# Kernel tuning notes

Hardware: AMD Instinct MI355X
Metric: run time of the kernel (lower is better)

## Reference

```python
import jax, jax.numpy as jnp
import numpy as np

N_NODES = 50000
N_EDGES = 800000
F_IN = 32
H = 128
N_REL = 4
MAX_DEG = 10
N_GRAPHS = 64
N_BLOCKS = 2


def setup_inputs() -> dict:
    key = jax.random.key(0)
    ks = jax.random.split(key, 20)
    s = 0.05
    return {
        "x": jax.random.normal(ks[0], (N_NODES, F_IN), jnp.float32),
        "edge_index": jax.random.randint(ks[1], (2, N_EDGES), 0, N_NODES, dtype=jnp.int32),
        "edge_attr": jax.random.randint(ks[2], (N_EDGES,), 0, N_REL, dtype=jnp.int32),
        "batch_idx": jnp.sort(jax.random.randint(ks[3], (N_NODES,), 0, N_GRAPHS, dtype=jnp.int32)),
        "embed_W": jax.random.normal(ks[4], (F_IN, H), jnp.float32) * s,
        "embed_b": jax.random.normal(ks[5], (H,), jnp.float32) * s,
        "rgcn_Wrel": jax.random.normal(ks[6], (N_BLOCKS, N_REL, H, H), jnp.float32) * s,
        "rgcn_Wroot": jax.random.normal(ks[7], (N_BLOCKS, H, H), jnp.float32) * s,
        "rgcn_b": jax.random.normal(ks[8], (N_BLOCKS, H), jnp.float32) * s,
        "mf_Wl": jax.random.normal(ks[9], (N_BLOCKS, MAX_DEG + 1, H, H), jnp.float32) * s,
        "mf_bl": jax.random.normal(ks[10], (N_BLOCKS, MAX_DEG + 1, H), jnp.float32) * s,
        "mf_Wr": jax.random.normal(ks[11], (N_BLOCKS, MAX_DEG + 1, H, H), jnp.float32) * s,
        "lin1_W": jax.random.normal(ks[12], (H, H), jnp.float32) * s,
        "lin1_b": jax.random.normal(ks[13], (H,), jnp.float32) * s,
        "lin2_W": jax.random.normal(ks[14], (H, 1), jnp.float32) * s,
        "lin2_b": jax.random.normal(ks[15], (1,), jnp.float32) * s,
    }


def _rgcn(x, src, dst, rel, Wrel, Wroot, b):
    # PyG RGCNConv with default aggr='mean': per-relation mean over incoming
    # edges, then per-relation weight, plus root transform and bias.
    seg = dst * N_REL + rel  # composite segment id: (node, relation)
    agg = jax.ops.segment_sum(x[src], seg, num_segments=N_NODES * N_REL)
    cnt = jax.ops.segment_sum(jnp.ones((seg.shape[0],), x.dtype), seg,
                              num_segments=N_NODES * N_REL)
    agg = (agg / jnp.maximum(cnt, 1.0)[:, None]).reshape(N_NODES, N_REL, H)
    return jnp.einsum('nrh,rho->no', agg, Wrel) + x @ Wroot + b


def _mfconv(x, src, dst, Wl, bl, Wr):
    # PyG MFConv: sum-aggregate neighbors, then per-degree-bucket linear heads
    # (degree = in-degree clamped to MAX_DEG); lin_r applied to root x (no bias).
    h = jax.ops.segment_sum(x[src], dst, num_segments=N_NODES)  # [N,H]
    deg = jax.ops.segment_sum(jnp.ones((src.shape[0],), jnp.int32), dst,
                              num_segments=N_NODES)
    deg = jnp.minimum(deg, MAX_DEG)  # [N]
    # out_all: [D+1, N, H] candidate outputs, one per degree bucket
    out_all = (jnp.einsum('nh,dho->dno', h, Wl)
               + jnp.einsum('nh,dho->dno', x, Wr)
               + bl[:, None, :])
    return jnp.take_along_axis(out_all, deg[None, :, None], axis=0)[0]


def reference(x, edge_index, edge_attr, batch_idx, embed_W, embed_b,
              rgcn_Wrel, rgcn_Wroot, rgcn_b, mf_Wl, mf_bl, mf_Wr,
              lin1_W, lin1_b, lin2_W, lin2_b):
    src, dst = edge_index[0], edge_index[1]
    h = x @ embed_W + embed_b
    for blk in range(N_BLOCKS):
        if blk > 0:  # first block uses Identity instead of ReLU
            h = jax.nn.relu(h)
        h = _rgcn(h, src, dst, edge_attr, rgcn_Wrel[blk], rgcn_Wroot[blk], rgcn_b[blk])
        h = jax.nn.relu(h)
        h = _mfconv(h, src, dst, mf_Wl[blk], mf_bl[blk], mf_Wr[blk])
    g = jax.ops.segment_sum(h, batch_idx, num_segments=N_GRAPHS)  # global_add_pool
    g = jax.nn.relu(g @ lin1_W + lin1_b)
    return g @ lin2_W + lin2_b
```

## Files before the change

### kernel.cpp

```cpp
#include <hip/hip_runtime.h>
#include <hip/hip_bf16.h>

#define NRELS 4
#define MAXDEG 10
#define NBUCK 11
#define POOL_CHUNKS 8

typedef __attribute__((ext_vector_type(8))) short s16x8;
typedef __attribute__((ext_vector_type(4))) float f32x4;
typedef __attribute__((ext_vector_type(8))) unsigned short u16x8;

__device__ inline unsigned short f2b(float f) {
  __hip_bfloat16 h = __float2bfloat16(f);
  return *reinterpret_cast<unsigned short*>(&h);
}
__device__ inline float b2f(unsigned short u) {
  union { unsigned int i; float f; } v;
  v.i = ((unsigned int)u) << 16;
  return v.f;
}
__device__ inline float blo(unsigned int v) {
  union { unsigned int i; float f; } x;
  x.i = v << 16;
  return x.f;
}
__device__ inline float bhi(unsigned int v) {
  union { unsigned int i; float f; } x;
  x.i = v & 0xffff0000u;
  return x.f;
}

typedef __attribute__((address_space(3))) unsigned int lds_uint;
typedef __attribute__((address_space(1))) const unsigned int glob_uint;
__device__ __forceinline__ void gld_lds16(const void* g, void* l) {
  __builtin_amdgcn_global_load_lds((glob_uint*)g, (lds_uint*)l, 16, 0, 0);
}

__global__ __launch_bounds__(512) void coarse_count(const int* __restrict__ dst,
                                                    int* __restrict__ bhist, int E) {
  __shared__ int lh[512];
  int t = threadIdx.x;
  lh[t] = 0;
  __syncthreads();
  int base = blockIdx.x * 4096;
  int lim = E - base;
  if (lim > 4096) lim = 4096;
  for (int i = t; i < lim; i += 512) atomicAdd(&lh[dst[base + i] >> 7], 1);
  __syncthreads();
  if (lh[t]) atomicAdd(&bhist[t], lh[t]);
}

__global__ __launch_bounds__(512) void coarse_scan(const int* __restrict__ bhist,
                                                   int* __restrict__ boff,
                                                   int* __restrict__ bcur, int NB, int E) {
  __shared__ int sd[512];
  int t = threadIdx.x;
  int v = (t < NB) ? bhist[t] : 0;
  sd[t] = v;
  __syncthreads();
  for (int o = 1; o < 512; o <<= 1) {
    int x = (t >= o) ? sd[t - o] : 0;
    __syncthreads();
    sd[t] += x;
    __syncthreads();
  }
  if (t < NB) {
    int st = sd[t] - v;
    boff[t] = st;
    bcur[t] = st;
  }
  if (t == 0) boff[NB] = E;
}

__global__ __launch_bounds__(512) void coarse_scatter(
    const int* __restrict__ src, const int* __restrict__ dst, const int* __restrict__ rel,
    int* __restrict__ bcur, uint2* __restrict__ ebuf, int E) {
  __shared__ int lhist[512];
  __shared__ int lstart[512];
  __shared__ int lcur[512];
  __shared__ int gbase[512];
  __shared__ uint2 stage[4096];
  int t = threadIdx.x;
  lhist[t] = 0;
  __syncthreads();
  int base = blockIdx.x * 4096;
  int lim = E - base;
  if (lim > 4096) lim = 4096;
  for (int i = t; i < lim; i += 512) atomicAdd(&lhist[dst[base + i] >> 7], 1);
  __syncthreads();
  int myc = lhist[t];
  lstart[t] = myc;
  __syncthreads();
  for (int o = 1; o < 512; o <<= 1) {
    int x = (t >= o) ? lstart[t - o] : 0;
    __syncthreads();
    lstart[t] += x;
    __syncthreads();
  }
  int incl = lstart[t];
  __syncthreads();
  lstart[t] = incl - myc;
  lcur[t] = 0;
  if (myc > 0) gbase[t] = atomicAdd(&bcur[t], myc);
  __syncthreads();
  for (int i = t; i < lim; i += 512) {
    int e = base + i;
    int d = dst[e];
    int b = d >> 7;
    int slot = lstart[b] + atomicAdd(&lcur[b], 1);
    stage[slot] = make_uint2((unsigned)(d * 4 + rel[e]), (unsigned)src[e]);
  }
  __syncthreads();
  for (int i = t; i < lim; i += 512) {
    uint2 val = stage[i];
    int b = (int)(val.x >> 9);
    ebuf[gbase[b] + (i - lstart[b])] = val;
  }
}

__global__ __launch_bounds__(512) void fine_count(const uint2* __restrict__ ebuf,
                                                  const int* __restrict__ boff,
                                                  int* __restrict__ cnt, int NSEG) {
  __shared__ int lh[512];
  int t = threadIdx.x;
  int b = blockIdx.x;
  lh[t] = 0;
  __syncthreads();
  int s = boff[b], e = boff[b + 1];
  for (int i = s + t; i < e; i += 512) atomicAdd(&lh[ebuf[i].x & 511], 1);
  __syncthreads();
  int gseg = b * 512 + t;
  if (gseg < NSEG) cnt[gseg] = lh[t];
}

__global__ __launch_bounds__(512) void place_local(const uint2* __restrict__ ebuf,
                                                   const int* __restrict__ boff,
                                                   const int* __restrict__ seg_start,
                                                   int* __restrict__ csr, int NSEG) {
  __shared__ int lcur[512];
  int t = threadIdx.x;
  int b = blockIdx.x;
  int gseg = b * 512 + t;
  lcur[t] = (gseg < NSEG) ? seg_start[gseg] : 0;
  __syncthreads();
  int s = boff[b], e = boff[b + 1];
  for (int i = s + t; i < e; i += 512) {
    uint2 v = ebuf[i];
    int pos = atomicAdd(&lcur[v.x & 511], 1);
    csr[pos] = (int)v.y;
  }
}

__global__ void prep_nodes(const int* __restrict__ cnt, float* __restrict__ inv,
                           int* __restrict__ deg, int* __restrict__ bucket,
                           int* __restrict__ hist, int N) {
  int n = blockIdx.x * 256 + threadIdx.x;
  int b = -1;
  if (n < N) {
    int d = 0;
    for (int r = 0; r < 4; r++) {
      int c = cnt[n * 4 + r];
      d += c;
      inv[n * 4 + r] = 1.0f / (float)(c > 1 ? c : 1);
    }
    deg[n] = d;
    b = d < MAXDEG ? d : MAXDEG;
    bucket[n] = b;
  }
  int lane = threadIdx.x & 63;
  for (int bb = 0; bb < NBUCK; bb++) {
    unsigned long long m = __ballot(b == bb);
    if (m == 0ULL) continue;
    int leader = __ffsll(m) - 1;
    if (lane == leader) atomicAdd(&hist[bb], __popcll(m));
  }
}

__global__ void calc_offsets(const int* __restrict__ hist, int* __restrict__ off,
                             int* __restrict__ fill) {
  if (threadIdx.x == 0) {
    int acc = 0;
    for (int b = 0; b < NBUCK; b++) {
      off[b] = acc;
      fill[b] = acc;
      acc += ((hist[b] + 63) >> 6) << 6;
    }
    off[NBUCK] = acc;
  }
}

__global__ void build_perm(const int* __restrict__ bucket, int* __restrict__ fill,
                           int* __restrict__ perm, int N) {
  int n = blockIdx.x * 256 + threadIdx.x;
  int b = (n < N) ? bucket[n] : -1;
  int lane = threadIdx.x & 63;
  for (int bb = 0; bb < NBUCK; bb++) {
    unsigned long long m = __ballot(b == bb);
    if (m == 0ULL) continue;
    int leader = __ffsll(m) - 1;
    int base = 0;
    if (lane == leader) base = atomicAdd(&fill[bb], __popcll(m));
    base = __shfl(base, leader);
    if (b == bb) {
      int idx = __popcll(m & ((1ULL << lane) - 1ULL));
      perm[base + idx] = n;
    }
  }
}

__global__ void assign_segments(const int* __restrict__ cnt, int* __restrict__ seg_start,
                                int* __restrict__ cursor, int NSEG) {
  __shared__ int sd[256];
  __shared__ int sbase;
  int t = threadIdx.x;
  int s = blockIdx.x * 256 + t;
  int v = (s < NSEG) ? cnt[s] : 0;
  sd[t] = v;
  __syncthreads();
  for (int o = 1; o < 256; o <<= 1) {
    int x = (t >= o) ? sd[t - o] : 0;
    __syncthreads();
    sd[t] += x;
    __syncthreads();
  }
  if (t == 255) sbase = atomicAdd(cursor, sd[255]);
  __syncthreads();
  if (s < NSEG) seg_start[s] = sbase + sd[t] - v;
}

__global__ void conv_weights(const float* __restrict__ Wrel, const float* __restrict__ Wroot,
                             const float* __restrict__ Wl, const float* __restrict__ Wr,
                             unsigned short* __restrict__ Bt, unsigned short* __restrict__ Btm) {
  int t = blockIdx.x * 256 + threadIdx.x;
  if (t < 2 * 128 * 640) {
    int blk = t / 81920;
    int rem = t % 81920;
    int n = rem / 640;
    int k = rem % 640;
    float v;
    if (k < 512)
      v = Wrel[(size_t)blk * 65536 + (size_t)k * 128 + n];
    else
      v = Wroot[(size_t)blk * 16384 + (size_t)(k - 512) * 128 + n];
    Bt[t] = f2b(v);
    return;
  }
  int t2 = t - 2 * 128 * 640;
  if (t2 >= 2 * 11 * 128 * 256) return;
  int k = t2 & 255;
  int n = (t2 >> 8) & 127;
  int bb = (t2 >> 15) % 11;
  int blk = t2 / (11 * 128 * 256);
  float v;
  if (k < 128)
    v = Wl[(((size_t)blk * 11 + bb) * 128 + k) * 128 + n];
  else
    v = Wr[(((size_t)blk * 11 + bb) * 128 + (k - 128)) * 128 + n];
  Btm[t2] = f2b(v);
}

#define ACC8(v)                                   \
  do {                                            \
    a0 += blo((v).x); a1 += bhi((v).x);           \
    a2 += blo((v).y); a3 += bhi((v).y);           \
    a4 += blo((v).z); a5 += bhi((v).z);           \
    a6 += blo((v).w); a7 += bhi((v).w);           \
  } while (0)

__global__ __launch_bounds__(256) void rgcn_gather(
    const unsigned short* __restrict__ hb, const int* __restrict__ csr,
    const int* __restrict__ seg_start, const int* __restrict__ cnt,
    const float* __restrict__ inv, unsigned short* __restrict__ ahat, int N) {
  int n = blockIdx.x * 16 + (threadIdx.x >> 4);
  if (n >= N) return;
  int c8 = (threadIdx.x & 15) * 8;
#pragma unroll
  for (int r = 0; r < 4; r++) {
    int seg = n * 4 + r;
    int st = seg_start[seg], cn = cnt[seg];
    float w = inv[seg];
    float a0 = 0.f, a1 = 0.f, a2 = 0.f, a3 = 0.f, a4 = 0.f, a5 = 0.f, a6 = 0.f, a7 = 0.f;
    int i = 0;
    for (; i + 4 <= cn; i += 4) {
      int p0 = csr[st + i], p1 = csr[st + i + 1];
      int p2 = csr[st + i + 2], p3 = csr[st + i + 3];
      uint4 v0 = *(const uint4*)(hb + (size_t)p0 * 128 + c8);
      uint4 v1 = *(const uint4*)(hb + (size_t)p1 * 128 + c8);
      uint4 v2 = *(const uint4*)(hb + (size_t)p2 * 128 + c8);
      uint4 v3 = *(const uint4*)(hb + (size_t)p3 * 128 + c8);
      ACC8(v0);
      ACC8(v1);
      ACC8(v2);
      ACC8(v3);
    }
    if (i + 2 <= cn) {
      int p0 = csr[st + i], p1 = csr[st + i + 1];
      uint4 v0 = *(const uint4*)(hb + (size_t)p0 * 128 + c8);
      uint4 v1 = *(const uint4*)(hb + (size_t)p1 * 128 + c8);
      ACC8(v0);
      ACC8(v1);
      i += 2;
    }
    if (i < cn) {
      uint4 v0 = *(const uint4*)(hb + (size_t)csr[st + i] * 128 + c8);
      ACC8(v0);
    }
    uint4 o;
    o.x = (unsigned int)f2b(a0 * w) | ((unsigned int)f2b(a1 * w) << 16);
    o.y = (unsigned int)f2b(a2 * w) | ((unsigned int)f2b(a3 * w) << 16);
    o.z = (unsigned int)f2b(a4 * w) | ((unsigned int)f2b(a5 * w) << 16);
    o.w = (unsigned int)f2b(a6 * w) | ((unsigned int)f2b(a7 * w) << 16);
    *(uint4*)(ahat + (size_t)n * 512 + r * 128 + c8) = o;
  }
}

__global__ __launch_bounds__(256) void mf_gather(
    const unsigned short* __restrict__ hb, const int* __restrict__ csr,
    const int* __restrict__ seg_start, const int* __restrict__ deg,
    const int* __restrict__ perm, unsigned short* __restrict__ amf, int total) {
  int i = blockIdx.x * 16 + (threadIdx.x >> 4);
  if (i >= total) return;
  int c8 = (threadIdx.x & 15) * 8;
  int n = perm[i];
  if (n < 0) return;
  int st = seg_start[n * 4], dg = deg[n];
  float a0 = 0.f, a1 = 0.f, a2 = 0.f, a3 = 0.f, a4 = 0.f, a5 = 0.f, a6 = 0.f, a7 = 0.f;
  int i2 = 0;
  for (; i2 + 4 <= dg; i2 += 4) {
    int p0 = csr[st + i2], p1 = csr[st + i2 + 1];
    int p2 = csr[st + i2 + 2], p3 = csr[st + i2 + 3];
    uint4 v0 = *(const uint4*)(hb + (size_t)p0 * 128 + c8);
    uint4 v1 = *(const uint4*)(hb + (size_t)p1 * 128 + c8);
    uint4 v2 = *(const uint4*)(hb + (size_t)p2 * 128 + c8);
    uint4 v3 = *(const uint4*)(hb + (size_t)p3 * 128 + c8);
    ACC8(v0);
    ACC8(v1);
    ACC8(v2);
    ACC8(v3);
  }
  if (i2 + 2 <= dg) {
    int p0 = csr[st + i2], p1 = csr[st + i2 + 1];
    uint4 v0 = *(const uint4*)(hb + (size_t)p0 * 128 + c8);
    uint4 v1 = *(const uint4*)(hb + (size_t)p1 * 128 + c8);
    ACC8(v0);
    ACC8(v1);
    i2 += 2;
  }
  if (i2 < dg) {
    uint4 v0 = *(const uint4*)(hb + (size_t)csr[st + i2] * 128 + c8);
    ACC8(v0);
  }
  uint4 o;
  o.x = (unsigned int)f2b(a0) | ((unsigned int)f2b(a1) << 16);
  o.y = (unsigned int)f2b(a2) | ((unsigned int)f2b(a3) << 16);
  o.z = (unsigned int)f2b(a4) | ((unsigned int)f2b(a5) << 16);
  o.w = (unsigned int)f2b(a6) | ((unsigned int)f2b(a7) << 16);
  *(uint4*)(amf + (size_t)i * 128 + c8) = o;
}

__global__ __launch_bounds__(256) void rgcn_mfma(const unsigned short* __restrict__ A,
                                                 const unsigned short* __restrict__ hroot,
                                                 const unsigned short* __restrict__ Bt,
                                                 const float* __restrict__ bias,
                                                 unsigned short* __restrict__ out, int N) {
  __shared__ unsigned char As[8192];
  __shared__ unsigned char Bs[16384];
  int t = threadIdx.x;
  int lane = t & 63, wave = t >> 6;
  int row = lane & 15, quad = lane >> 4;
  int m0 = blockIdx.x * 64;
  int nh = wave * 32;
  f32x4 acc[2][4];
#pragma unroll
  for (int i = 0; i < 2; i++)
#pragma unroll
    for (int j = 0; j < 4; j++) acc[i][j] = (f32x4){0.f, 0.f, 0.f, 0.f};

  for (int kt = 0; kt < 10; kt++) {
    int kb2 = kt * 128;
#pragma unroll
    for (int s = 0; s < 2; s++) {
      int o = s * 4096 + t * 16;
      int r = o >> 7, c = ((o >> 4) & 7) ^ (r & 7);
      int gr = m0 + r;
      if (gr >= N) gr = N - 1;
      const char* gsrc = (kt < 8) ? ((const char*)A + (size_t)gr * 1024 + kb2 + c * 16)
                                  : ((const char*)hroot + (size_t)gr * 256 + (kb2 - 1024) + c * 16);
      gld_lds16(gsrc, As + o);
    }
#pragma unroll
    for (int s = 0; s < 4; s++) {
      int o = s * 4096 + t * 16;
      int r = o >> 7, c = ((o >> 4) & 7) ^ (r & 7);
      gld_lds16((const char*)Bt + (size_t)r * 1280 + kb2 + c * 16, Bs + o);
    }
    __syncthreads();
#pragma unroll
    for (int ks = 0; ks < 2; ks++) {
      int cch = ks * 4 + quad;
      s16x8 af[4], bf[2];
#pragma unroll
      for (int mt = 0; mt < 4; mt++) {
        int R = mt * 16 + row;
        af[mt] = *(const s16x8*)(As + R * 128 + ((cch ^ (R & 7)) << 4));
      }
#pragma unroll
      for (int nt = 0; nt < 2; nt++) {
        int R = nh + nt * 16 + row;
        bf[nt] = *(const s16x8*)(Bs + R * 128 + ((cch ^ (R & 7)) << 4));
      }
#pragma unroll
      for (int nt = 0; nt < 2; nt++)
#pragma unroll
        for (int mt = 0; mt < 4; mt++)
          acc[nt][mt] = __builtin_amdgcn_mfma_f32_16x16x32_bf16(af[mt], bf[nt], acc[nt][mt], 0, 0, 0);
    }
    __syncthreads();
  }
#pragma unroll
  for (int nt = 0; nt < 2; nt++) {
    int n = nh + nt * 16 + row;
    float bv = bias[n];
#pragma unroll
    for (int mt = 0; mt < 4; mt++) {
#pragma unroll
      for (int r4 = 0; r4 < 4; r4++) {
        int m = m0 + mt * 16 + quad * 4 + r4;
        if (m < N) out[(size_t)m * 128 + n] = f2b(fmaxf(acc[nt][mt][r4] + bv, 0.f));
      }
    }
  }
}

__global__ __launch_bounds__(256) void mf_mfma(const unsigned short* __restrict__ A,
                                               const unsigned short* __restrict__ hroot,
                                               const unsigned short* __restrict__ Bt,
                                               const float* __restrict__ bl,
                                               const int* __restrict__ perm,
                                               const int* __restrict__ off,
                                               unsigned short* __restrict__ out, int relu_out) {
  __shared__ unsigned char As[8192];
  __shared__ unsigned char Bs[16384];
  __shared__ int soff[12];
  __shared__ int nodes[64];
  int t = threadIdx.x;
  int m0 = blockIdx.x * 64;
  if (t < 12) soff[t] = off[t];
  if (t >= 64 && t < 128) nodes[t - 64] = perm[m0 + t - 64];
  __syncthreads();
  if (m0 >= soff[11]) return;
  int b = 0;
  while (b < 10 && m0 >= soff[b + 1]) b++;
  const unsigned short* Bb = Bt + (size_t)b * 128 * 256;
  const float* bb = bl + b * 128;
  int lane = t & 63, wave = t >> 6;
  int row = lane & 15, quad = lane >> 4;
  int nh = wave * 32;
  f32x4 acc[2][4];
#pragma unroll
  for (int i = 0; i < 2; i++)
#pragma unroll
    for (int j = 0; j < 4; j++) acc[i][j] = (f32x4){0.f, 0.f, 0.f, 0.f};

  for (int kt = 0; kt < 4; kt++) {
    int kb2 = kt * 128;
#pragma unroll
    for (int s = 0; s < 2; s++) {
      int o = s * 4096 + t * 16;
      int r = o >> 7, c = ((o >> 4) & 7) ^ (r & 7);
      const char* gsrc;
      if (kt < 2) {
        gsrc = (const char*)A + (size_t)(m0 + r) * 256 + kb2 + c * 16;
      } else {
        int nd = nodes[r];
        if (nd < 0) nd = 0;
        gsrc = (const char*)hroot + (size_t)nd * 256 + (kb2 - 512) + c * 16;
      }
      gld_lds16(gsrc, As + o);
    }
#pragma unroll
    for (int s = 0; s < 4; s++) {
      int o = s * 4096 + t * 16;
      int r = o >> 7, c = ((o >> 4) & 7) ^ (r & 7);
      gld_lds16((const char*)Bb + (size_t)r * 512 + kb2 + c * 16, Bs + o);
    }
    __syncthreads();
#pragma unroll
    for (int ks = 0; ks < 2; ks++) {
      int cch = ks * 4 + quad;
      s16x8 af[4], bf[2];
#pragma unroll
      for (int mt = 0; mt < 4; mt++) {
        int R = mt * 16 + row;
        af[mt] = *(const s16x8*)(As + R * 128 + ((cch ^ (R & 7)) << 4));
      }
#pragma unroll
      for (int nt = 0; nt < 2; nt++) {
        int R = nh + nt * 16 + row;
        bf[nt] = *(const s16x8*)(Bs + R * 128 + ((cch ^ (R & 7)) << 4));
      }
#pragma unroll
      for (int nt = 0; nt < 2; nt++)
#pragma unroll
        for (int mt = 0; mt < 4; mt++)
          acc[nt][mt] = __builtin_amdgcn_mfma_f32_16x16x32_bf16(af[mt], bf[nt], acc[nt][mt], 0, 0, 0);
    }
    __syncthreads();
  }
#pragma unroll
  for (int nt = 0; nt < 2; nt++) {
    int n = nh + nt * 16 + row;
    float bv = bb[n];
#pragma unroll
    for (int mt = 0; mt < 4; mt++) {
#pragma unroll
      for (int r4 = 0; r4 < 4; r4++) {
        int nd = nodes[mt * 16 + quad * 4 + r4];
        if (nd >= 0) {
          float v = acc[nt][mt][r4] + bv;
          if (relu_out) v = fmaxf(v, 0.f);
          out[(size_t)nd * 128 + n] = f2b(v);
        }
      }
    }
  }
}

__global__ __launch_bounds__(256) void embed_gemm(const float* __restrict__ x,
                                                  const float* __restrict__ W,
                                                  const float* __restrict__ bias,
                                                  unsigned short* __restrict__ out, int N) {
  __shared__ float As[64][33];
  __shared__ float Ws[32][128];
  int tid = threadIdx.x;
  int row0 = blockIdx.x * 64;
  int tx = tid & 15, ty = tid >> 4;
  int tx8 = tx * 8, ty4 = ty * 4;
  float acc[4][8];
#pragma unroll
  for (int j = 0; j < 8; j++) {
    float bv = bias[tx8 + j];
#pragma unroll
    for (int i = 0; i < 4; i++) acc[i][j] = bv;
  }
#pragma unroll
  for (int l = 0; l < 8; l++) {
    int lin = tid + l * 256;
    int r = lin >> 5, kk = lin & 31;
    int n = row0 + r;
    As[r][kk] = (n < N) ? x[(size_t)n * 32 + kk] : 0.f;
  }
#pragma unroll
  for (int l = 0; l < 16; l++) {
    int lin = tid + l * 256;
    Ws[lin >> 7][lin & 127] = W[lin];
  }
  __syncthreads();
#pragma unroll
  for (int kk = 0; kk < 32; kk++) {
    float a[4];
#pragma unroll
    for (int i = 0; i < 4; i++) a[i] = As[ty4 + i][kk];
    float4 w0 = *(const float4*)&Ws[kk][tx8];
    float4 w1 = *(const float4*)&Ws[kk][tx8 + 4];
    float w[8] = {w0.x, w0.y, w0.z, w0.w, w1.x, w1.y, w1.z, w1.w};
#pragma unroll
    for (int i = 0; i < 4; i++)
#pragma unroll
      for (int j = 0; j < 8; j++) acc[i][j] += a[i] * w[j];
  }
#pragma unroll
  for (int i = 0; i < 4; i++) {
    int n = row0 + ty4 + i;
    if (n < N) {
      u16x8 o;
#pragma unroll
      for (int j = 0; j < 8; j++) o[j] = f2b(acc[i][j]);
      *(u16x8*)&out[(size_t)n * 128 + tx8] = o;
    }
  }
}

__global__ void pool2(const unsigned short* __restrict__ h, const int* __restrict__ batch,
                      float* __restrict__ g, int N, int G) {
  int gr = blockIdx.x / POOL_CHUNKS;
  int ck = blockIdx.x % POOL_CHUNKS;
  int c = threadIdx.x;
  int lo = 0, hi = N;
  while (lo < hi) {
    int m = (lo + hi) >> 1;
    if (batch[m] < gr) lo = m + 1; else hi = m;
  }
  int s = lo;
  lo = s; hi = N;
  while (lo < hi) {
    int m = (lo + hi) >> 1;
    if (batch[m] < gr + 1) lo = m + 1; else hi = m;
  }
  int e = lo;
  int len = e - s;
  int a = s + (int)(((long long)len * ck) / POOL_CHUNKS);
  int b = s + (int)(((long long)len * (ck + 1)) / POOL_CHUNKS);
  float sum = 0.f;
  for (int n = a; n < b; n++) sum += b2f(h[(size_t)n * 128 + c]);
  if (b > a) atomicAdd(&g[gr * 128 + c], sum);
}

__global__ void head_kernel(const float* __restrict__ g, const float* __restrict__ W1,
                            const float* __restrict__ b1, const float* __restrict__ W2,
                            const float* __restrict__ b2, float* __restrict__ out) {
  int bg = blockIdx.x;
  int o = threadIdx.x;
  __shared__ float gs[128];
  __shared__ float red[128];
  gs[o] = g[bg * 128 + o];
  __syncthreads();
  float acc = b1[o];
  for (int k = 0; k < 128; k++) acc += gs[k] * W1[k * 128 + o];
  acc = fmaxf(acc, 0.f);
  red[o] = acc * W2[o];
  __syncthreads();
  for (int s = 64; s > 0; s >>= 1) {
    if (o < s) red[o] += red[o + s];
    __syncthreads();
  }
  if (o == 0) out[bg] = red[0] + b2[0];
}

extern "C" void kernel_launch(void* const* d_in, const int* in_sizes, int n_in,
                              void* d_out, int out_size, void* d_ws, size_t ws_size,
                              hipStream_t stream) {
  const float* x = (const float*)d_in[0];
  const int* ei = (const int*)d_in[1];
  const int* ea = (const int*)d_in[2];
  const int* batch = (const int*)d_in[3];
  const float* embW = (const float*)d_in[4];
  const float* embB = (const float*)d_in[5];
  const float* Wrel = (const float*)d_in[6];
  const float* Wroot = (const float*)d_in[7];
  const float* rb = (const float*)d_in[8];
  const float* Wl = (const float*)d_in[9];
  const float* bl = (const float*)d_in[10];
  const float* Wr = (const float*)d_in[11];
  const float* l1W = (const float*)d_in[12];
  const float* l1b = (const float*)d_in[13];
  const float* l2W = (const float*)d_in[14];
  const float* l2b = (const float*)d_in[15];
  float* out = (float*)d_out;

  int N = in_sizes[0] / 32;
  int E = in_sizes[2];
  int G = out_size;
  int NSEG = N * 4;
  int NB = (N + 127) >> 7;

  char* p = (char*)d_ws;
  auto alloc = [&](size_t bytes) {
    char* r = p;
    p += (bytes + 255) & ~(size_t)255;
    return r;
  };
  int permCap = ((N + 63) / 64 + NBUCK) * 64;
  unsigned short* h_bf = (unsigned short*)alloc((size_t)N * 128 * 2);
  unsigned short* h2_bf = (unsigned short*)alloc((size_t)N * 128 * 2);
  unsigned short* ahat = (unsigned short*)alloc((size_t)N * 512 * 2);
  unsigned short* amf = (unsigned short*)alloc((size_t)permCap * 128 * 2);
  unsigned short* Btr = (unsigned short*)alloc((size_t)2 * 128 * 640 * 2);
  unsigned short* Btm = (unsigned short*)alloc((size_t)2 * 11 * 128 * 256 * 2);
  float* inv = (float*)alloc((size_t)NSEG * 4);
  int* cnt = (int*)alloc((size_t)NSEG * 4);
  int* seg_start = (int*)alloc((size_t)NSEG * 4);
  int* csr = (int*)alloc((size_t)E * 4);
  uint2* ebuf = (uint2*)alloc((size_t)E * 8);
  int* deg = (int*)alloc((size_t)N * 4);
  int* bucket = (int*)alloc((size_t)N * 4);
  int* perm = (int*)alloc((size_t)permCap * 4);
  int* bhist = (int*)alloc(512 * 4);
  int* boff = (int*)alloc(516 * 4);
  int* bcur = (int*)alloc(512 * 4);
  int* hist = (int*)alloc(64);
  int* off = (int*)alloc(64);
  int* fill = (int*)alloc(64);
  int* cursor = (int*)alloc(64);
  float* g = (float*)alloc((size_t)G * 128 * 4);

  hipMemsetAsync(bhist, 0, 512 * 4, stream);
  hipMemsetAsync(hist, 0, 64, stream);
  hipMemsetAsync(cursor, 0, 64, stream);
  hipMemsetAsync(g, 0, (size_t)G * 128 * 4, stream);
  hipMemsetAsync(perm, 0xFF, (size_t)permCap * 4, stream);

  const int* src = ei;
  const int* dst = ei + E;

  int sblocks = (E + 4095) / 4096;
  coarse_count<<<sblocks, 512, 0, stream>>>(dst, bhist, E);
  coarse_scan<<<1, 512, 0, stream>>>(bhist, boff, bcur, NB, E);
  coarse_scatter<<<sblocks, 512, 0, stream>>>(src, dst, ea, bcur, ebuf, E);
  fine_count<<<NB, 512, 0, stream>>>(ebuf, boff, cnt, NSEG);
  prep_nodes<<<(N + 255) / 256, 256, 0, stream>>>(cnt, inv, deg, bucket, hist, N);
  calc_offsets<<<1, 64, 0, stream>>>(hist, off, fill);
  build_perm<<<(N + 255) / 256, 256, 0, stream>>>(bucket, fill, perm, N);
  assign_segments<<<(NSEG + 255) / 256, 256, 0, stream>>>(cnt, seg_start, cursor, NSEG);
  place_local<<<NB, 512, 0, stream>>>(ebuf, boff, seg_start, csr, NSEG);
  int convTotal = 2 * 128 * 640 + 2 * 11 * 128 * 256;
  conv_weights<<<(convTotal + 255) / 256, 256, 0, stream>>>(Wrel, Wroot, Wl, Wr, Btr, Btm);

  embed_gemm<<<(N + 63) / 64, 256, 0, stream>>>(x, embW, embB, h_bf, N);

  int nb = (N + 63) / 64;
  int mfblocks = permCap / 64;
  for (int blk = 0; blk < 2; blk++) {
    rgcn_gather<<<(N + 15) / 16, 256, 0, stream>>>(h_bf, csr, seg_start, cnt, inv, ahat, N);
    rgcn_mfma<<<nb, 256, 0, stream>>>(ahat, h_bf, Btr + (size_t)blk * 81920, rb + blk * 128,
                                      h2_bf, N);
    mf_gather<<<(permCap + 15) / 16, 256, 0, stream>>>(h2_bf, csr, seg_start, deg, perm, amf,
                                                       permCap);
    mf_mfma<<<mfblocks, 256, 0, stream>>>(amf, h2_bf, Btm + (size_t)blk * 11 * 128 * 256,
                                          bl + (size_t)blk * 11 * 128, perm, off, h_bf,
                                          (blk == 0) ? 1 : 0);
  }
  pool2<<<G * POOL_CHUNKS, 128, 0, stream>>>(h_bf, batch, g, N, G);
  head_kernel<<<G, 128, 0, stream>>>(g, l1W, l1b, l2W, l2b, out);
}
```

Before: 467.8 us.

## Fuse node prep with segment scan and reorder RGCN gather by degree bucket

```diff
diff --git a/kernel.cpp b/kernel.cpp
--- a/kernel.cpp
+++ b/kernel.cpp
@@ -151,23 +151,36 @@
   }
 }
 
-__global__ void prep_nodes(const int* __restrict__ cnt, float* __restrict__ inv,
-                           int* __restrict__ deg, int* __restrict__ bucket,
-                           int* __restrict__ hist, int N) {
-  int n = blockIdx.x * 256 + threadIdx.x;
+__global__ __launch_bounds__(256) void prep_and_scan(
+    const int* __restrict__ cnt, float* __restrict__ inv, int* __restrict__ deg,
+    int* __restrict__ bucket, int* __restrict__ hist, int* __restrict__ seg_start,
+    int* __restrict__ cursor, int NSEG) {
+  __shared__ int sd[256];
+  __shared__ int sbase;
+  int t = threadIdx.x;
+  int s = blockIdx.x * 256 + t;
+  int v = (s < NSEG) ? cnt[s] : 0;
+  sd[t] = v;
+  if (s < NSEG) inv[s] = 1.0f / (float)(v > 1 ? v : 1);
+  __syncthreads();
+  for (int o = 1; o < 256; o <<= 1) {
+    int x = (t >= o) ? sd[t - o] : 0;
+    __syncthreads();
+    sd[t] += x;
+    __syncthreads();
+  }
+  if (t == 255) sbase = atomicAdd(cursor, sd[255]);
+  __syncthreads();
+  if (s < NSEG) seg_start[s] = sbase + sd[t] - v;
   int b = -1;
-  if (n < N) {
-    int d = 0;
-    for (int r = 0; r < 4; r++) {
-      int c = cnt[n * 4 + r];
-      d += c;
-      inv[n * 4 + r] = 1.0f / (float)(c > 1 ? c : 1);
-    }
+  if ((t & 3) == 0 && s < NSEG) {
+    int d = sd[t + 3] - sd[t] + v;
+    int n = s >> 2;
     deg[n] = d;
     b = d < MAXDEG ? d : MAXDEG;
     bucket[n] = b;
   }
-  int lane = threadIdx.x & 63;
+  int lane = t & 63;
   for (int bb = 0; bb < NBUCK; bb++) {
     unsigned long long m = __ballot(b == bb);
     if (m == 0ULL) continue;
@@ -206,26 +219,6 @@
       perm[base + idx] = n;
     }
   }
-}
-
-__global__ void assign_segments(const int* __restrict__ cnt, int* __restrict__ seg_start,
-                                int* __restrict__ cursor, int NSEG) {
-  __shared__ int sd[256];
-  __shared__ int sbase;
-  int t = threadIdx.x;
-  int s = blockIdx.x * 256 + t;
-  int v = (s < NSEG) ? cnt[s] : 0;
-  sd[t] = v;
-  __syncthreads();
-  for (int o = 1; o < 256; o <<= 1) {
-    int x = (t >= o) ? sd[t - o] : 0;
-    __syncthreads();
-    sd[t] += x;
-    __syncthreads();
-  }
-  if (t == 255) sbase = atomicAdd(cursor, sd[255]);
-  __syncthreads();
-  if (s < NSEG) seg_start[s] = sbase + sd[t] - v;
 }
 
 __global__ void conv_weights(const float* __restrict__ Wrel, const float* __restrict__ Wroot,
@@ -270,9 +263,12 @@
 __global__ __launch_bounds__(256) void rgcn_gather(
     const unsigned short* __restrict__ hb, const int* __restrict__ csr,
     const int* __restrict__ seg_start, const int* __restrict__ cnt,
-    const float* __restrict__ inv, unsigned short* __restrict__ ahat, int N) {
-  int n = blockIdx.x * 16 + (threadIdx.x >> 4);
-  if (n >= N) return;
+    const float* __restrict__ inv, const int* __restrict__ perm,
+    unsigned short* __restrict__ ahat, int total) {
+  int i = blockIdx.x * 16 + (threadIdx.x >> 4);
+  if (i >= total) return;
+  int n = perm[i];
+  if (n < 0) return;
   int c8 = (threadIdx.x & 15) * 8;
 #pragma unroll
   for (int r = 0; r < 4; r++) {
@@ -280,10 +276,10 @@
     int st = seg_start[seg], cn = cnt[seg];
     float w = inv[seg];
     float a0 = 0.f, a1 = 0.f, a2 = 0.f, a3 = 0.f, a4 = 0.f, a5 = 0.f, a6 = 0.f, a7 = 0.f;
-    int i = 0;
-    for (; i + 4 <= cn; i += 4) {
-      int p0 = csr[st + i], p1 = csr[st + i + 1];
-      int p2 = csr[st + i + 2], p3 = csr[st + i + 3];
+    int ii = 0;
+    for (; ii + 4 <= cn; ii += 4) {
+      int p0 = csr[st + ii], p1 = csr[st + ii + 1];
+      int p2 = csr[st + ii + 2], p3 = csr[st + ii + 3];
       uint4 v0 = *(const uint4*)(hb + (size_t)p0 * 128 + c8);
       uint4 v1 = *(const uint4*)(hb + (size_t)p1 * 128 + c8);
       uint4 v2 = *(const uint4*)(hb + (size_t)p2 * 128 + c8);
@@ -293,16 +289,16 @@
       ACC8(v2);
       ACC8(v3);
     }
-    if (i + 2 <= cn) {
-      int p0 = csr[st + i], p1 = csr[st + i + 1];
+    if (ii + 2 <= cn) {
+      int p0 = csr[st + ii], p1 = csr[st + ii + 1];
       uint4 v0 = *(const uint4*)(hb + (size_t)p0 * 128 + c8);
       uint4 v1 = *(const uint4*)(hb + (size_t)p1 * 128 + c8);
       ACC8(v0);
       ACC8(v1);
-      i += 2;
-    }
-    if (i < cn) {
-      uint4 v0 = *(const uint4*)(hb + (size_t)csr[st + i] * 128 + c8);
+      ii += 2;
+    }
+    if (ii < cn) {
+      uint4 v0 = *(const uint4*)(hb + (size_t)csr[st + ii] * 128 + c8);
       ACC8(v0);
     }
     uint4 o;
@@ -310,7 +306,7 @@
     o.y = (unsigned int)f2b(a2 * w) | ((unsigned int)f2b(a3 * w) << 16);
     o.z = (unsigned int)f2b(a4 * w) | ((unsigned int)f2b(a5 * w) << 16);
     o.w = (unsigned int)f2b(a6 * w) | ((unsigned int)f2b(a7 * w) << 16);
-    *(uint4*)(ahat + (size_t)n * 512 + r * 128 + c8) = o;
+    *(uint4*)(ahat + (size_t)i * 512 + r * 128 + c8) = o;
   }
 }
 
@@ -362,13 +358,17 @@
                                                  const unsigned short* __restrict__ hroot,
                                                  const unsigned short* __restrict__ Bt,
                                                  const float* __restrict__ bias,
-                                                 unsigned short* __restrict__ out, int N) {
+                                                 const int* __restrict__ perm,
+                                                 unsigned short* __restrict__ out) {
   __shared__ unsigned char As[8192];
   __shared__ unsigned char Bs[16384];
+  __shared__ int nodes[64];
   int t = threadIdx.x;
+  int m0 = blockIdx.x * 64;
+  if (t >= 64 && t < 128) nodes[t - 64] = perm[m0 + t - 64];
+  __syncthreads();
   int lane = t & 63, wave = t >> 6;
   int row = lane & 15, quad = lane >> 4;
-  int m0 = blockIdx.x * 64;
   int nh = wave * 32;
   f32x4 acc[2][4];
 #pragma unroll
@@ -382,10 +382,14 @@
     for (int s = 0; s < 2; s++) {
       int o = s * 4096 + t * 16;
       int r = o >> 7, c = ((o >> 4) & 7) ^ (r & 7);
-      int gr = m0 + r;
-      if (gr >= N) gr = N - 1;
-      const char* gsrc = (kt < 8) ? ((const char*)A + (size_t)gr * 1024 + kb2 + c * 16)
-                                  : ((const char*)hroot + (size_t)gr * 256 + (kb2 - 1024) + c * 16);
+      const char* gsrc;
+      if (kt < 8) {
+        gsrc = (const char*)A + (size_t)(m0 + r) * 1024 + kb2 + c * 16;
+      } else {
+        int nd = nodes[r];
+        if (nd < 0) nd = 0;
+        gsrc = (const char*)hroot + (size_t)nd * 256 + (kb2 - 1024) + c * 16;
+      }
       gld_lds16(gsrc, As + o);
     }
 #pragma unroll
@@ -425,8 +429,8 @@
     for (int mt = 0; mt < 4; mt++) {
 #pragma unroll
       for (int r4 = 0; r4 < 4; r4++) {
-        int m = m0 + mt * 16 + quad * 4 + r4;
-        if (m < N) out[(size_t)m * 128 + n] = f2b(fmaxf(acc[nt][mt][r4] + bv, 0.f));
+        int nd = nodes[mt * 16 + quad * 4 + r4];
+        if (nd >= 0) out[(size_t)nd * 128 + n] = f2b(fmaxf(acc[nt][mt][r4] + bv, 0.f));
       }
     }
   }
@@ -663,7 +667,7 @@
   int permCap = ((N + 63) / 64 + NBUCK) * 64;
   unsigned short* h_bf = (unsigned short*)alloc((size_t)N * 128 * 2);
   unsigned short* h2_bf = (unsigned short*)alloc((size_t)N * 128 * 2);
-  unsigned short* ahat = (unsigned short*)alloc((size_t)N * 512 * 2);
+  unsigned short* ahat = (unsigned short*)alloc((size_t)permCap * 512 * 2);
   unsigned short* amf = (unsigned short*)alloc((size_t)permCap * 128 * 2);
   unsigned short* Btr = (unsigned short*)alloc((size_t)2 * 128 * 640 * 2);
   unsigned short* Btm = (unsigned short*)alloc((size_t)2 * 11 * 128 * 256 * 2);
@@ -675,19 +679,18 @@
   int* deg = (int*)alloc((size_t)N * 4);
   int* bucket = (int*)alloc((size_t)N * 4);
   int* perm = (int*)alloc((size_t)permCap * 4);
-  int* bhist = (int*)alloc(512 * 4);
   int* boff = (int*)alloc(516 * 4);
   int* bcur = (int*)alloc(512 * 4);
-  int* hist = (int*)alloc(64);
   int* off = (int*)alloc(64);
   int* fill = (int*)alloc(64);
-  int* cursor = (int*)alloc(64);
-  float* g = (float*)alloc((size_t)G * 128 * 4);
-
-  hipMemsetAsync(bhist, 0, 512 * 4, stream);
-  hipMemsetAsync(hist, 0, 64, stream);
-  hipMemsetAsync(cursor, 0, 64, stream);
-  hipMemsetAsync(g, 0, (size_t)G * 128 * 4, stream);
+  size_t zeroBytes = 512 * 4 + 64 + 64 + (size_t)G * 128 * 4;
+  char* zb = alloc(zeroBytes);
+  int* bhist = (int*)zb;
+  int* hist = (int*)(zb + 2048);
+  int* cursor = (int*)(zb + 2048 + 64);
+  float* g = (float*)(zb + 2048 + 128);
+
+  hipMemsetAsync(zb, 0, zeroBytes, stream);
   hipMemsetAsync(perm, 0xFF, (size_t)permCap * 4, stream);
 
   const int* src = ei;
@@ -698,22 +701,22 @@
   coarse_scan<<<1, 512, 0, stream>>>(bhist, boff, bcur, NB, E);
   coarse_scatter<<<sblocks, 512, 0, stream>>>(src, dst, ea, bcur, ebuf, E);
   fine_count<<<NB, 512, 0, stream>>>(ebuf, boff, cnt, NSEG);
-  prep_nodes<<<(N + 255) / 256, 256, 0, stream>>>(cnt, inv, deg, bucket, hist, N);
+  prep_and_scan<<<(NSEG + 255) / 256, 256, 0, stream>>>(cnt, inv, deg, bucket, hist,
+                                                        seg_start, cursor, NSEG);
   calc_offsets<<<1, 64, 0, stream>>>(hist, off, fill);
   build_perm<<<(N + 255) / 256, 256, 0, stream>>>(bucket, fill, perm, N);
-  assign_segments<<<(NSEG + 255) / 256, 256, 0, stream>>>(cnt, seg_start, cursor, NSEG);
   place_local<<<NB, 512, 0, stream>>>(ebuf, boff, seg_start, csr, NSEG);
   int convTotal = 2 * 128 * 640 + 2 * 11 * 128 * 256;
   conv_weights<<<(convTotal + 255) / 256, 256, 0, stream>>>(Wrel, Wroot, Wl, Wr, Btr, Btm);
 
   embed_gemm<<<(N + 63) / 64, 256, 0, stream>>>(x, embW, embB, h_bf, N);
 
-  int nb = (N + 63) / 64;
   int mfblocks = permCap / 64;
   for (int blk = 0; blk < 2; blk++) {
-    rgcn_gather<<<(N + 15) / 16, 256, 0, stream>>>(h_bf, csr, seg_start, cnt, inv, ahat, N);
-    rgcn_mfma<<<nb, 256, 0, stream>>>(ahat, h_bf, Btr + (size_t)blk * 81920, rb + blk * 128,
-                                      h2_bf, N);
+    rgcn_gather<<<(permCap + 15) / 16, 256, 0, stream>>>(h_bf, csr, seg_start, cnt, inv, perm,
+                                                         ahat, permCap);
+    rgcn_mfma<<<mfblocks, 256, 0, stream>>>(ahat, h_bf, Btr + (size_t)blk * 81920,
+                                            rb + blk * 128, perm, h2_bf);
     mf_gather<<<(permCap + 15) / 16, 256, 0, stream>>>(h2_bf, csr, seg_start, deg, perm, amf,
                                                        permCap);
     mf_mfma<<<mfblocks, 256, 0, stream>>>(amf, h2_bf, Btm + (size_t)blk * 11 * 128 * 256,
```

Result: slower. 492.8 us (+5.3%).
